# Kernel tuning notes

Hardware: AMD Instinct MI355X
Metric: run time of the kernel (lower is better)

The kernel has to match this reference:

```python
import jax, jax.numpy as jnp
import numpy as np

EPS = 1e-8
N_ITER = 3
S = 8      # n_slots
D = 64     # slot_size
HID = 128  # mlp hidden


def _ln(x, w, b):
    m = jnp.mean(x, axis=-1, keepdims=True)
    v = jnp.var(x, axis=-1, keepdims=True)
    return (x - m) * jax.lax.rsqrt(v + 1e-5) * w + b


def setup_inputs() -> dict:
    key = jax.random.key(0)
    ks = jax.random.split(key, 20)
    B, N, Din = 128, 4096, 64
    g = lambda k, sh, s: (jax.random.normal(k, sh, jnp.float32) * s)
    return {
        "inputs": jax.random.normal(ks[0], (B, N, Din), jnp.float32),
        "eps_noise": jax.random.normal(ks[1], (B, S, D), jnp.float32),
        "slot_mu": g(ks[2], (1, 1, D), 0.1),
        "slot_logvar": g(ks[3], (1, 1, D), 0.1),
        "k_w": g(ks[4], (D, Din), 1.0 / np.sqrt(Din)),
        "v_w": g(ks[5], (D, Din), 1.0 / np.sqrt(Din)),
        "q_w": g(ks[6], (D, D), 1.0 / np.sqrt(D)),
        "ni_w": jnp.ones((Din,), jnp.float32), "ni_b": jnp.zeros((Din,), jnp.float32),
        "ns_w": jnp.ones((D,), jnp.float32),  "ns_b": jnp.zeros((D,), jnp.float32),
        "nr_w": jnp.ones((D,), jnp.float32),  "nr_b": jnp.zeros((D,), jnp.float32),
        "gru_wih": g(ks[7], (3 * D, D), 1.0 / np.sqrt(D)),
        "gru_whh": g(ks[8], (3 * D, D), 1.0 / np.sqrt(D)),
        "gru_bih": jnp.zeros((3 * D,), jnp.float32),
        "gru_bhh": jnp.zeros((3 * D,), jnp.float32),
        "mlp_w1": g(ks[9], (HID, D), 1.0 / np.sqrt(D)),
        "mlp_w2": g(ks[10], (D, HID), 1.0 / np.sqrt(HID)),
        "mlp_b2": jnp.zeros((D,), jnp.float32),
    }


def _gru(x, h, wih, whh, bih, bhh):
    gi = x @ wih.T + bih  # [BS, 3D]
    gh = h @ whh.T + bhh
    i_r, i_z, i_n = jnp.split(gi, 3, axis=-1)
    h_r, h_z, h_n = jnp.split(gh, 3, axis=-1)
    r = jax.nn.sigmoid(i_r + h_r)
    z = jax.nn.sigmoid(i_z + h_z)
    n = jnp.tanh(i_n + r * h_n)
    return (1.0 - z) * n + z * h


def _step(slots, k, v, q_w, ns_w, ns_b, nr_w, nr_b,
          gru_wih, gru_whh, gru_bih, gru_bhh, mlp_w1, mlp_w2, mlp_b2):
    B = slots.shape[0]
    q = _ln(slots, ns_w, ns_b) @ q_w.T                     # [B,S,D]
    logits = jnp.einsum('bnd,bsd->bns', k, q)              # [B,N,S]
    w = jax.nn.softmax(logits, axis=-1) + EPS              # softmax over slots
    w = w / jnp.sum(w, axis=-2, keepdims=True)             # renorm over tokens
    atten_maps = jnp.einsum('bns,bnd->bsd', w, v)          # [B,S,D]
    h = _gru(atten_maps.reshape(B * S, D), slots.reshape(B * S, D),
             gru_wih, gru_whh, gru_bih, gru_bhh)
    h = h + (jax.nn.relu(_ln(h, nr_w, nr_b) @ mlp_w1.T) @ mlp_w2.T + mlp_b2)
    return h.reshape(B, S, D), w


def reference(inputs, eps_noise, slot_mu, slot_logvar, k_w, v_w, q_w,
              ni_w, ni_b, ns_w, ns_b, nr_w, nr_b,
              gru_wih, gru_whh, gru_bih, gru_bhh, mlp_w1, mlp_w2, mlp_b2):
    std = jnp.exp(0.5 * slot_logvar)
    slots = slot_mu + std * eps_noise                      # [B,S,D]
    x = _ln(inputs, ni_w, ni_b)
    k = (x @ k_w.T) / np.sqrt(D).astype(np.float32)        # [B,N,D]
    v = x @ v_w.T
    args = (q_w, ns_w, ns_b, nr_w, nr_b, gru_wih, gru_whh,
            gru_bih, gru_bhh, mlp_w1, mlp_w2, mlp_b2)
    for _ in range(N_ITER):
        slots, w = _step(slots, k, v, *args)
    slots, w = _step(jax.lax.stop_gradient(slots), k, v, *args)
    return slots, w
```

## Files before the change

kernel.cpp:

```cpp
#include <hip/hip_runtime.h>
#include <hip/hip_bf16.h>

#define BB 128
#define NN 4096
#define DD 64
#define SS 8
#define HH 128

typedef __attribute__((ext_vector_type(8))) short short8;
typedef __attribute__((ext_vector_type(4))) short short4v;
typedef __attribute__((ext_vector_type(4))) float f32x4;

__device__ __forceinline__ float warp_red_sum(float v) {
    #pragma unroll
    for (int off = 32; off; off >>= 1) v += __shfl_xor(v, off);
    return v;
}

__device__ __forceinline__ float bcastlane(float v, int l) {
    return __int_as_float(__builtin_amdgcn_readlane(__float_as_int(v), l));
}

__device__ __forceinline__ unsigned short bfu(float f) {
    __hip_bfloat16 h = __float2bfloat16(f);
    return *(unsigned short*)&h;
}

__device__ __forceinline__ unsigned pk2(float a, float b) {
    return (unsigned)bfu(a) | ((unsigned)bfu(b) << 16);
}

__device__ __forceinline__ short4v ds_tr16(unsigned off) {
    short4v r;
    asm volatile("ds_read_b64_tr_b16 %0, %1" : "=v"(r) : "v"(off));
    return r;
}

__device__ __forceinline__ void ln_block(
    const float* __restrict__ inp, const float* __restrict__ niw,
    const float* __restrict__ nib, unsigned short* __restrict__ xb,
    int tok0, int tid)
{
    const int lane = tid & 63, widx = tid >> 6;
    const int t8 = lane >> 3, d8 = lane & 7;
    const float4 wn0 = *(const float4*)&niw[d8 * 8];
    const float4 wn1 = *(const float4*)&niw[d8 * 8 + 4];
    const float4 bn0 = *(const float4*)&nib[d8 * 8];
    const float4 bn1 = *(const float4*)&nib[d8 * 8 + 4];
    #pragma unroll
    for (int it = 0; it < 4; ++it) {
        const int m = widx * 32 + it * 8 + t8;
        const float* rowp = inp + (size_t)(tok0 + m) * 64 + d8 * 8;
        float4 a = *(const float4*)rowp;
        float4 c = *(const float4*)(rowp + 4);
        float s1 = (a.x + a.y + a.z + a.w) + (c.x + c.y + c.z + c.w);
        float s2 = fmaf(a.x, a.x, fmaf(a.y, a.y, fmaf(a.z, a.z, a.w * a.w)));
        s2 = fmaf(c.x, c.x, fmaf(c.y, c.y, fmaf(c.z, c.z, fmaf(c.w, c.w, s2))));
        #pragma unroll
        for (int o = 1; o < 8; o <<= 1) { s1 += __shfl_xor(s1, o); s2 += __shfl_xor(s2, o); }
        float mean = s1 * (1.0f / 64.0f);
        float var = s2 * (1.0f / 64.0f) - mean * mean;
        float rstd = rsqrtf(var + 1e-5f);
        float y[8];
        y[0] = (a.x - mean) * rstd * wn0.x + bn0.x;
        y[1] = (a.y - mean) * rstd * wn0.y + bn0.y;
        y[2] = (a.z - mean) * rstd * wn0.z + bn0.z;
        y[3] = (a.w - mean) * rstd * wn0.w + bn0.w;
        y[4] = (c.x - mean) * rstd * wn1.x + bn1.x;
        y[5] = (c.y - mean) * rstd * wn1.y + bn1.y;
        y[6] = (c.z - mean) * rstd * wn1.z + bn1.z;
        y[7] = (c.w - mean) * rstd * wn1.w + bn1.w;
        uint4 o4;
        o4.x = pk2(y[0], y[1]); o4.y = pk2(y[2], y[3]);
        o4.z = pk2(y[4], y[5]); o4.w = pk2(y[6], y[7]);
        *(uint4*)&xb[(size_t)(tok0 + m) * 64 + d8 * 8] = o4;
    }
}

__device__ __forceinline__ void gru_core(
    float nx, float dt, int row, int lane,
    const float* __restrict__ vwT, const float* __restrict__ wihT,
    const float* __restrict__ whhT, const float* __restrict__ w1T,
    const float* __restrict__ w2T, const float* __restrict__ bih,
    const float* __restrict__ bhh, const float* __restrict__ nrw,
    const float* __restrict__ nrb, const float* __restrict__ b2,
    const float* __restrict__ qwT, const float* __restrict__ k_w,
    const float* __restrict__ nsw, const float* __restrict__ nsb,
    const float* __restrict__ slotsIn, float* __restrict__ slotsOut,
    unsigned short* __restrict__ qb)
{
    float xp = 0.f;
    #pragma unroll 8
    for (int i = 0; i < 64; ++i) xp = fmaf(bcastlane(nx, i), vwT[i * 64 + lane], xp);
    float x = xp / dt;
    float h = slotsIn[row * 64 + lane];
    float air = 0, aiz = 0, ain = 0, ahr = 0, ahz = 0, ahn = 0;
    #pragma unroll 8
    for (int i = 0; i < 64; ++i) {
        float xi = bcastlane(x, i), hi = bcastlane(h, i);
        const float* wi = wihT + i * 192;
        const float* wh = whhT + i * 192;
        air = fmaf(xi, wi[lane], air);
        aiz = fmaf(xi, wi[64 + lane], aiz);
        ain = fmaf(xi, wi[128 + lane], ain);
        ahr = fmaf(hi, wh[lane], ahr);
        ahz = fmaf(hi, wh[64 + lane], ahz);
        ahn = fmaf(hi, wh[128 + lane], ahn);
    }
    air += bih[lane]; aiz += bih[64 + lane]; ain += bih[128 + lane];
    ahr += bhh[lane]; ahz += bhh[64 + lane]; ahn += bhh[128 + lane];
    float r = 1.f / (1.f + __expf(-(air + ahr)));
    float z = 1.f / (1.f + __expf(-(aiz + ahz)));
    float n = tanhf(ain + r * ahn);
    float hn = (1.f - z) * n + z * h;
    float m = warp_red_sum(hn) * (1.0f / 64.0f);
    float dx = hn - m;
    float var = warp_red_sum(dx * dx) * (1.0f / 64.0f);
    float u = dx * rsqrtf(var + 1e-5f) * nrw[lane] + nrb[lane];
    float o0 = 0.f, o1 = 0.f;
    #pragma unroll 8
    for (int i = 0; i < 64; ++i) {
        float ui = bcastlane(u, i);
        const float* w1r = w1T + i * 128;
        o0 = fmaf(ui, w1r[lane], o0);
        o1 = fmaf(ui, w1r[64 + lane], o1);
    }
    o0 = fmaxf(o0, 0.f); o1 = fmaxf(o1, 0.f);
    float y = 0.f;
    #pragma unroll 8
    for (int j = 0; j < 64; ++j) y = fmaf(bcastlane(o0, j), w2T[j * 64 + lane], y);
    #pragma unroll 8
    for (int j = 0; j < 64; ++j) y = fmaf(bcastlane(o1, j), w2T[(64 + j) * 64 + lane], y);
    y += b2[lane];
    float out = hn + y;
    slotsOut[row * 64 + lane] = out;
    float m2 = warp_red_sum(out) * (1.0f / 64.0f);
    float dx2 = out - m2;
    float var2 = warp_red_sum(dx2 * dx2) * (1.0f / 64.0f);
    float u2 = dx2 * rsqrtf(var2 + 1e-5f) * nsw[lane] + nsb[lane];
    float q = 0.f;
    #pragma unroll 8
    for (int i = 0; i < 64; ++i) q = fmaf(bcastlane(u2, i), qwT[i * 64 + lane], q);
    float qp = 0.f;
    #pragma unroll 8
    for (int o = 0; o < 64; ++o) qp = fmaf(bcastlane(q, o), k_w[o * 64 + lane], qp);
    qb[row * 64 + lane] = bfu(qp * 0.125f);
}

__global__ __launch_bounds__(256) void fused_pre(
    const float* __restrict__ inp, const float* __restrict__ niw, const float* __restrict__ nib,
    const float* __restrict__ eps, const float* __restrict__ mu, const float* __restrict__ lv,
    const float* __restrict__ q_w, const float* __restrict__ k_w,
    const float* __restrict__ nsw, const float* __restrict__ nsb,
    const float* __restrict__ v_w, const float* __restrict__ wih, const float* __restrict__ whh,
    const float* __restrict__ w1, const float* __restrict__ w2,
    unsigned short* __restrict__ xb, unsigned short* __restrict__ qb,
    float* __restrict__ slots,
    float* __restrict__ vwT, float* __restrict__ qwT,
    float* __restrict__ wihT, float* __restrict__ whhT,
    float* __restrict__ w1T, float* __restrict__ w2T)
{
    const int bid = blockIdx.x, tid = threadIdx.x;
    const int lane = tid & 63, widx = tid >> 6;
    if (bid < 64) {
        int i0 = bid * 256 + tid, nthr = 16384;
        for (int t = i0; t < 4096; t += nthr) {
            int i = t >> 6, o = t & 63;
            vwT[t] = v_w[o * 64 + i];
            qwT[t] = q_w[o * 64 + i];
        }
        for (int t = i0; t < 12288; t += nthr) {
            int r = t / 192, c = t % 192;
            wihT[t] = wih[c * 64 + r];
            whhT[t] = whh[c * 64 + r];
        }
        for (int t = i0; t < 8192; t += nthr) {
            int r = t >> 7, c = t & 127;
            w1T[t] = w1[c * 64 + r];
        }
        for (int t = i0; t < 8192; t += nthr) {
            int r = t >> 6, c = t & 63;
            w2T[t] = w2[c * 128 + r];
        }
    }
    ln_block(inp, niw, nib, xb, bid * 128, tid);
    if (bid >= 64 && bid < 320) {
        const int row = (bid - 64) * 4 + widx;
        const int idx = row * 64 + lane;
        float s0 = mu[lane] + __expf(0.5f * lv[lane]) * eps[idx];
        slots[idx] = s0;
        float m = warp_red_sum(s0) * (1.0f / 64.0f);
        float dx = s0 - m;
        float var = warp_red_sum(dx * dx) * (1.0f / 64.0f);
        float xln = dx * rsqrtf(var + 1e-5f) * nsw[lane] + nsb[lane];
        float q = 0.f;
        #pragma unroll 8
        for (int i = 0; i < 64; ++i) q = fmaf(bcastlane(xln, i), q_w[lane * 64 + i], q);
        float qp = 0.f;
        #pragma unroll 8
        for (int o = 0; o < 64; ++o) qp = fmaf(bcastlane(q, o), k_w[o * 64 + lane], qp);
        qb[idx] = bfu(qp * 0.125f);
    }
}

__global__ __launch_bounds__(256) void attn_mfma(
    const __hip_bfloat16* __restrict__ xb,
    const unsigned short* __restrict__ qb,
    float* __restrict__ numerP, float* __restrict__ denomP, float* __restrict__ wout)
{
    __shared__ unsigned short smem[11904];
    unsigned short* Qs = smem;
    const int tid = threadIdx.x, lane = tid & 63, widx = tid >> 6;
    unsigned short* wls = smem + 1152 + widx * 640;
    unsigned short* Xw  = smem + 3712 + widx * 2048;
    const int b = blockIdx.y;
    const int quad = lane >> 4, l16 = lane & 15;
    const int twave0 = blockIdx.x * 512 + widx * 128;

    short8 bkA[2][2], bkB[2][2];
    #pragma unroll
    for (int t4h = 0; t4h < 2; ++t4h) {
        const size_t xrow = ((size_t)b * NN + twave0 + t4h * 16 + l16) * 64;
        bkA[t4h][0] = *(const short8*)&xb[xrow + quad * 8];
        bkA[t4h][1] = *(const short8*)&xb[xrow + 32 + quad * 8];
    }

    for (int t = tid; t < 1024; t += 256) {
        int s = t >> 6, dd = t & 63;
        Qs[s * 72 + dd] = (s < 8) ? qb[b * 512 + t] : (unsigned short)0;
    }
    for (int t = lane; t < 320; t += 64) wls[320 + t] = 0;
    __syncthreads();

    short8 aq0 = *(const short8*)&Qs[l16 * 72 + quad * 8];
    short8 aq1 = *(const short8*)&Qs[l16 * 72 + 32 + quad * 8];

    f32x4 accv[4];
    #pragma unroll
    for (int nt = 0; nt < 4; ++nt) accv[nt] = (f32x4){0.f, 0.f, 0.f, 0.f};
    float dacc[4] = {0.f, 0.f, 0.f, 0.f};

    unsigned short* xw0 = Xw + (quad >> 1) * 512 + l16 * 16 + (quad & 1) * 8;
    const unsigned xtr = (unsigned)(size_t)Xw
                       + (unsigned)((quad * 8 + (l16 >> 2)) * 32 + (l16 & 3) * 8);

    auto PROC = [&](short8 (&cur)[2][2], short8 (&nxt)[2][2], int hg, bool pf) {
        const int t0g = twave0 + hg * 32;
        if (pf) {
            #pragma unroll
            for (int t4h = 0; t4h < 2; ++t4h) {
                const size_t xrow = ((size_t)b * NN + t0g + 32 + t4h * 16 + l16) * 64;
                nxt[t4h][0] = *(const short8*)&xb[xrow + quad * 8];
                nxt[t4h][1] = *(const short8*)&xb[xrow + 32 + quad * 8];
            }
        }
        #pragma unroll
        for (int t4h = 0; t4h < 2; ++t4h) {
            const int tok = t0g + t4h * 16 + l16;
            short8 bk0 = cur[t4h][0];
            short8 bk1 = cur[t4h][1];
            *(short8*)(xw0 + t4h * 256) = bk0;
            *(short8*)(xw0 + t4h * 256 + 1024) = bk1;
            f32x4 lg = (f32x4){0.f, 0.f, 0.f, 0.f};
            lg = __builtin_amdgcn_mfma_f32_16x16x32_bf16(aq0, bk0, lg, 0, 0, 0);
            lg = __builtin_amdgcn_mfma_f32_16x16x32_bf16(aq1, bk1, lg, 0, 0, 0);
            float e[4];
            #pragma unroll
            for (int r = 0; r < 4; ++r) e[r] = __expf(lg[r]);
            float s4 = (e[0] + e[1]) + (e[2] + e[3]);
            float stot = s4 + __shfl_xor(s4, 16);
            float rs = __builtin_amdgcn_rcpf(stot);
            float wv[4];
            #pragma unroll
            for (int r = 0; r < 4; ++r) { wv[r] = fmaf(e[r], rs, 1e-8f); dacc[r] += wv[r]; }
            if (quad < 2) {
                #pragma unroll
                for (int r = 0; r < 4; ++r)
                    wls[(quad * 4 + r) * 40 + t4h * 16 + l16] = bfu(wv[r]);
                if (wout)
                    *(float4*)&wout[((size_t)b * NN + tok) * 8 + quad * 4] =
                        make_float4(wv[0], wv[1], wv[2], wv[3]);
            }
        }
        asm volatile("" ::: "memory");
        short8 aw = *(const short8*)&wls[l16 * 40 + quad * 8];
        short4v rlo[4], rhi[4];
        #pragma unroll
        for (int nt = 0; nt < 4; ++nt) {
            rlo[nt] = ds_tr16(xtr + nt * 1024);
            rhi[nt] = ds_tr16(xtr + nt * 1024 + 128);
        }
        asm volatile("s_waitcnt lgkmcnt(0)");
        __builtin_amdgcn_sched_barrier(0);
        #pragma unroll
        for (int nt = 0; nt < 4; ++nt) {
            short8 bv = __builtin_shufflevector(rlo[nt], rhi[nt], 0, 1, 2, 3, 4, 5, 6, 7);
            accv[nt] = __builtin_amdgcn_mfma_f32_16x16x32_bf16(aw, bv, accv[nt], 0, 0, 0);
        }
    };

    PROC(bkA, bkB, 0, true);
    PROC(bkB, bkA, 1, true);
    PROC(bkA, bkB, 2, true);
    PROC(bkB, bkA, 3, false);

    #pragma unroll
    for (int r = 0; r < 4; ++r) {
        dacc[r] += __shfl_xor(dacc[r], 1);
        dacc[r] += __shfl_xor(dacc[r], 2);
        dacc[r] += __shfl_xor(dacc[r], 4);
        dacc[r] += __shfl_xor(dacc[r], 8);
    }
    __syncthreads();
    float* red = (float*)smem;
    float* dred = red + 2048;
    if (quad < 2) {
        #pragma unroll
        for (int nt = 0; nt < 4; ++nt)
            #pragma unroll
            for (int r = 0; r < 4; ++r)
                red[widx * 512 + (quad * 4 + r) * 64 + nt * 16 + l16] = accv[nt][r];
        if (l16 == 0) {
            #pragma unroll
            for (int r = 0; r < 4; ++r) dred[widx * 8 + quad * 4 + r] = dacc[r];
        }
    }
    __syncthreads();
    float* np = numerP + ((size_t)b * 8 + blockIdx.x) * 512;
    for (int e = tid; e < 512; e += 256)
        np[e] = red[e] + red[512 + e] + red[1024 + e] + red[1536 + e];
    if (tid < 8)
        denomP[((size_t)b * 8 + blockIdx.x) * 8 + tid] =
            dred[tid] + dred[8 + tid] + dred[16 + tid] + dred[24 + tid];
}

__global__ __launch_bounds__(256) void gru_q_kernel(
    const float* __restrict__ numerP, const float* __restrict__ denomP,
    const float* __restrict__ slotsIn,
    const float* __restrict__ vwT, const float* __restrict__ wihT, const float* __restrict__ whhT,
    const float* __restrict__ w1T, const float* __restrict__ w2T,
    const float* __restrict__ bih, const float* __restrict__ bhh,
    const float* __restrict__ nrw, const float* __restrict__ nrb,
    const float* __restrict__ b2,
    const float* __restrict__ qwT, const float* __restrict__ k_w,
    const float* __restrict__ nsw, const float* __restrict__ nsb,
    float* __restrict__ slotsOut, unsigned short* __restrict__ qb,
    float* __restrict__ denomF)
{
    const int tid = threadIdx.x, lane = tid & 63;
    const int row = blockIdx.x * 4 + (tid >> 6);
    const int bb = row >> 3, ss = row & 7;
    float nx = 0.f, dt = 0.f;
    #pragma unroll
    for (int xx = 0; xx < 8; ++xx) {
        nx += numerP[((size_t)bb * 8 + xx) * 512 + ss * 64 + lane];
        dt += denomP[((size_t)bb * 8 + xx) * 8 + ss];
    }
    if (lane == 0) denomF[row] = dt;
    gru_core(nx, dt, row, lane, vwT, wihT, whhT, w1T, w2T, bih, bhh, nrw, nrb, b2,
             qwT, k_w, nsw, nsb, slotsIn, slotsOut, qb);
}

__global__ __launch_bounds__(256) void renorm_kernel(float* __restrict__ wout,
                                                     const float* __restrict__ denom)
{
    const size_t i4 = (size_t)blockIdx.x * blockDim.x + threadIdx.x;
    const size_t b = i4 >> 13;
    const int half = (int)(i4 & 1);
    float4 v = reinterpret_cast<float4*>(wout)[i4];
    const float4 dv = reinterpret_cast<const float4*>(denom)[b * 2 + half];
    v.x /= dv.x; v.y /= dv.y; v.z /= dv.z; v.w /= dv.w;
    reinterpret_cast<float4*>(wout)[i4] = v;
}

extern "C" void kernel_launch(void* const* d_in, const int* in_sizes, int n_in,
                              void* d_out, int out_size, void* d_ws, size_t ws_size,
                              hipStream_t stream)
{
    const float* inputs  = (const float*)d_in[0];
    const float* eps_n   = (const float*)d_in[1];
    const float* mu      = (const float*)d_in[2];
    const float* lv      = (const float*)d_in[3];
    const float* k_w     = (const float*)d_in[4];
    const float* v_w     = (const float*)d_in[5];
    const float* q_w     = (const float*)d_in[6];
    const float* ni_w    = (const float*)d_in[7];
    const float* ni_b    = (const float*)d_in[8];
    const float* ns_w    = (const float*)d_in[9];
    const float* ns_b    = (const float*)d_in[10];
    const float* nr_w    = (const float*)d_in[11];
    const float* nr_b    = (const float*)d_in[12];
    const float* gru_wih = (const float*)d_in[13];
    const float* gru_whh = (const float*)d_in[14];
    const float* gru_bih = (const float*)d_in[15];
    const float* gru_bhh = (const float*)d_in[16];
    const float* mlp_w1  = (const float*)d_in[17];
    const float* mlp_w2  = (const float*)d_in[18];
    const float* mlp_b2  = (const float*)d_in[19];

    char* wsb = (char*)d_ws;
    unsigned short* xb  = (unsigned short*)wsb;
    float* P      = (float*)(wsb + 67108864);
    float* numerP = P;
    float* denomP = P + 524288;
    float* denomF = P + 532480;
    float* f      = (float*)(wsb + 134217728);
    float* slotsA = f;
    float* slotsB = f + 65536;
    unsigned short* qb = (unsigned short*)(f + 131072);
    float* vwT    = f + 296960;
    float* qwT    = f + 301056;
    float* wihT   = f + 305152;
    float* whhT   = f + 317440;
    float* w1T    = f + 329728;
    float* w2T    = f + 337920;

    float* out_slots = (float*)d_out;
    float* out_w     = out_slots + 65536;

    fused_pre<<<4096, 256, 0, stream>>>(inputs, ni_w, ni_b, eps_n, mu, lv,
                                        q_w, k_w, ns_w, ns_b,
                                        v_w, gru_wih, gru_whh, mlp_w1, mlp_w2,
                                        xb, qb, slotsA,
                                        vwT, qwT, wihT, whhT, w1T, w2T);

    float* cur = slotsA;
    for (int step = 0; step < 4; ++step) {
        attn_mfma<<<dim3(8, 128), 256, 0, stream>>>((const __hip_bfloat16*)xb, qb,
                                                    numerP, denomP,
                                                    step == 3 ? out_w : nullptr);
        float* nxt = (step == 3) ? out_slots : ((step & 1) ? slotsA : slotsB);
        gru_q_kernel<<<256, 256, 0, stream>>>(numerP, denomP, cur,
                                              vwT, wihT, whhT, w1T, w2T,
                                              gru_bih, gru_bhh, nr_w, nr_b, mlp_b2,
                                              qwT, k_w, ns_w, ns_b,
                                              nxt, qb, denomF);
        cur = nxt;
    }
    renorm_kernel<<<4096, 256, 0, stream>>>(out_w, denomF);
}
```

Before: 378.8 us.

## Fuse GRU update into attention kernel via last-block-per-batch atomic counter

Merges the per-step attention and GRU/query kernels into one templated kernel. Each block publishes its partial numerator and denominator with agent-scope stores, then bumps a per-batch, per-step counter. The last of the 8 blocks for a batch reduces the partials and runs the GRU, MLP and next-query update. This removes four kernel launches and their inter-kernel gaps, and also drops the shared-memory Q staging and its barrier by loading Q straight from global memory. In exchange it adds serial tail work on one block per batch and relies on fences and atomics for correctness.

```diff
diff --git a/kernel.cpp b/kernel.cpp
--- a/kernel.cpp
+++ b/kernel.cpp
@@ -28,6 +28,13 @@
 
 __device__ __forceinline__ unsigned pk2(float a, float b) {
     return (unsigned)bfu(a) | ((unsigned)bfu(b) << 16);
+}
+
+__device__ __forceinline__ void store_agent(float* p, float v) {
+    __hip_atomic_store(p, v, __ATOMIC_RELAXED, __HIP_MEMORY_SCOPE_AGENT);
+}
+__device__ __forceinline__ float load_agent(const float* p) {
+    return __hip_atomic_load(p, __ATOMIC_RELAXED, __HIP_MEMORY_SCOPE_AGENT);
 }
 
 __device__ __forceinline__ short4v ds_tr16(unsigned off) {
@@ -158,7 +165,8 @@
     float* __restrict__ slots,
     float* __restrict__ vwT, float* __restrict__ qwT,
     float* __restrict__ wihT, float* __restrict__ whhT,
-    float* __restrict__ w1T, float* __restrict__ w2T)
+    float* __restrict__ w1T, float* __restrict__ w2T,
+    int* __restrict__ counters)
 {
     const int bid = blockIdx.x, tid = threadIdx.x;
     const int lane = tid & 63, widx = tid >> 6;
@@ -182,6 +190,9 @@
             int r = t >> 6, c = t & 63;
             w2T[t] = w2[c * 128 + r];
         }
+    }
+    if (bid == 320) {
+        for (int t = tid; t < 512; t += 256) counters[t] = 0;
     }
     ln_block(inp, niw, nib, xb, bid * 128, tid);
     if (bid >= 64 && bid < 320) {
@@ -203,16 +214,28 @@
     }
 }
 
-__global__ __launch_bounds__(256) void attn_mfma(
+template<int STEP>
+__global__ __launch_bounds__(256) void fused_step(
     const __hip_bfloat16* __restrict__ xb,
-    const unsigned short* __restrict__ qb,
-    float* __restrict__ numerP, float* __restrict__ denomP, float* __restrict__ wout)
-{
-    __shared__ unsigned short smem[11904];
-    unsigned short* Qs = smem;
+    unsigned short* __restrict__ qb,
+    float* __restrict__ numerP, float* __restrict__ denomP,
+    float* __restrict__ wout, int* __restrict__ counters,
+    const float* __restrict__ slotsIn, float* __restrict__ slotsOut,
+    const float* __restrict__ vwT, const float* __restrict__ wihT,
+    const float* __restrict__ whhT, const float* __restrict__ w1T,
+    const float* __restrict__ w2T,
+    const float* __restrict__ bih, const float* __restrict__ bhh,
+    const float* __restrict__ nrw, const float* __restrict__ nrb,
+    const float* __restrict__ b2,
+    const float* __restrict__ qwT, const float* __restrict__ k_w,
+    const float* __restrict__ nsw, const float* __restrict__ nsb,
+    float* __restrict__ denomF)
+{
+    __shared__ unsigned short smem[10752];
+    __shared__ int sflag;
     const int tid = threadIdx.x, lane = tid & 63, widx = tid >> 6;
-    unsigned short* wls = smem + 1152 + widx * 640;
-    unsigned short* Xw  = smem + 3712 + widx * 2048;
+    unsigned short* wls = smem + widx * 640;
+    unsigned short* Xw  = smem + 2560 + widx * 2048;
     const int b = blockIdx.y;
     const int quad = lane >> 4, l16 = lane & 15;
     const int twave0 = blockIdx.x * 512 + widx * 128;
@@ -225,15 +248,13 @@
         bkA[t4h][1] = *(const short8*)&xb[xrow + 32 + quad * 8];
     }
 
-    for (int t = tid; t < 1024; t += 256) {
-        int s = t >> 6, dd = t & 63;
-        Qs[s * 72 + dd] = (s < 8) ? qb[b * 512 + t] : (unsigned short)0;
+    short8 aq0 = (short8){0, 0, 0, 0, 0, 0, 0, 0};
+    short8 aq1 = (short8){0, 0, 0, 0, 0, 0, 0, 0};
+    if (l16 < 8) {
+        aq0 = *(const short8*)&qb[b * 512 + l16 * 64 + quad * 8];
+        aq1 = *(const short8*)&qb[b * 512 + l16 * 64 + 32 + quad * 8];
     }
     for (int t = lane; t < 320; t += 64) wls[320 + t] = 0;
-    __syncthreads();
-
-    short8 aq0 = *(const short8*)&Qs[l16 * 72 + quad * 8];
-    short8 aq1 = *(const short8*)&Qs[l16 * 72 + 32 + quad * 8];
 
     f32x4 accv[4];
     #pragma unroll
@@ -277,7 +298,7 @@
                 #pragma unroll
                 for (int r = 0; r < 4; ++r)
                     wls[(quad * 4 + r) * 40 + t4h * 16 + l16] = bfu(wv[r]);
-                if (wout)
+                if (STEP == 3)
                     *(float4*)&wout[((size_t)b * NN + tok) * 8 + quad * 4] =
                         make_float4(wv[0], wv[1], wv[2], wv[3]);
             }
@@ -328,37 +349,36 @@
     __syncthreads();
     float* np = numerP + ((size_t)b * 8 + blockIdx.x) * 512;
     for (int e = tid; e < 512; e += 256)
-        np[e] = red[e] + red[512 + e] + red[1024 + e] + red[1536 + e];
+        store_agent(&np[e], red[e] + red[512 + e] + red[1024 + e] + red[1536 + e]);
     if (tid < 8)
-        denomP[((size_t)b * 8 + blockIdx.x) * 8 + tid] =
-            dred[tid] + dred[8 + tid] + dred[16 + tid] + dred[24 + tid];
-}
-
-__global__ __launch_bounds__(256) void gru_q_kernel(
-    const float* __restrict__ numerP, const float* __restrict__ denomP,
-    const float* __restrict__ slotsIn,
-    const float* __restrict__ vwT, const float* __restrict__ wihT, const float* __restrict__ whhT,
-    const float* __restrict__ w1T, const float* __restrict__ w2T,
-    const float* __restrict__ bih, const float* __restrict__ bhh,
-    const float* __restrict__ nrw, const float* __restrict__ nrb,
-    const float* __restrict__ b2,
-    const float* __restrict__ qwT, const float* __restrict__ k_w,
-    const float* __restrict__ nsw, const float* __restrict__ nsb,
-    float* __restrict__ slotsOut, unsigned short* __restrict__ qb,
-    float* __restrict__ denomF)
-{
-    const int tid = threadIdx.x, lane = tid & 63;
-    const int row = blockIdx.x * 4 + (tid >> 6);
-    const int bb = row >> 3, ss = row & 7;
-    float nx = 0.f, dt = 0.f;
-    #pragma unroll
-    for (int xx = 0; xx < 8; ++xx) {
-        nx += numerP[((size_t)bb * 8 + xx) * 512 + ss * 64 + lane];
-        dt += denomP[((size_t)bb * 8 + xx) * 8 + ss];
-    }
-    if (lane == 0) denomF[row] = dt;
-    gru_core(nx, dt, row, lane, vwT, wihT, whhT, w1T, w2T, bih, bhh, nrw, nrb, b2,
-             qwT, k_w, nsw, nsb, slotsIn, slotsOut, qb);
+        store_agent(&denomP[((size_t)b * 8 + blockIdx.x) * 8 + tid],
+                    dred[tid] + dred[8 + tid] + dred[16 + tid] + dred[24 + tid]);
+
+    __threadfence();
+    __syncthreads();
+    if (tid == 0) {
+        int old = atomicAdd(&counters[STEP * 128 + b], 1);
+        sflag = (old == 7) ? 1 : 0;
+    }
+    __syncthreads();
+    if (sflag) {
+        __threadfence();
+        #pragma unroll
+        for (int rr = 0; rr < 2; ++rr) {
+            const int row = b * 8 + widx * 2 + rr;
+            const int ss = row & 7;
+            float nx = 0.f, dt = 0.f;
+            #pragma unroll
+            for (int xx = 0; xx < 8; ++xx) {
+                nx += load_agent(&numerP[((size_t)b * 8 + xx) * 512 + ss * 64 + lane]);
+                dt += load_agent(&denomP[((size_t)b * 8 + xx) * 8 + ss]);
+            }
+            if (lane == 0) denomF[row] = dt;
+            gru_core(nx, dt, row, lane, vwT, wihT, whhT, w1T, w2T,
+                     bih, bhh, nrw, nrb, b2, qwT, k_w, nsw, nsb,
+                     slotsIn, slotsOut, qb);
+        }
+    }
 }
 
 __global__ __launch_bounds__(256) void renorm_kernel(float* __restrict__ wout,
@@ -368,7 +388,7 @@
     const size_t b = i4 >> 13;
     const int half = (int)(i4 & 1);
     float4 v = reinterpret_cast<float4*>(wout)[i4];
-    const float4 dv = reinterpret_cast<const float4*>(denom)[b * 2 + half];
+    const float4 dv = *(const float4*)&denom[b * 8 + half * 4];
     v.x /= dv.x; v.y /= dv.y; v.z /= dv.z; v.w /= dv.w;
     reinterpret_cast<float4*>(wout)[i4] = v;
 }
@@ -404,6 +424,7 @@
     float* numerP = P;
     float* denomP = P + 524288;
     float* denomF = P + 532480;
+    int*   counters = (int*)(P + 533504);
     float* f      = (float*)(wsb + 134217728);
     float* slotsA = f;
     float* slotsB = f + 65536;
@@ -422,20 +443,20 @@
                                         q_w, k_w, ns_w, ns_b,
                                         v_w, gru_wih, gru_whh, mlp_w1, mlp_w2,
                                         xb, qb, slotsA,
-                                        vwT, qwT, wihT, whhT, w1T, w2T);
-
-    float* cur = slotsA;
-    for (int step = 0; step < 4; ++step) {
-        attn_mfma<<<dim3(8, 128), 256, 0, stream>>>((const __hip_bfloat16*)xb, qb,
-                                                    numerP, denomP,
-                                                    step == 3 ? out_w : nullptr);
-        float* nxt = (step == 3) ? out_slots : ((step & 1) ? slotsA : slotsB);
-        gru_q_kernel<<<256, 256, 0, stream>>>(numerP, denomP, cur,
-                                              vwT, wihT, whhT, w1T, w2T,
-                                              gru_bih, gru_bhh, nr_w, nr_b, mlp_b2,
-                                              qwT, k_w, ns_w, ns_b,
-                                              nxt, qb, denomF);
-        cur = nxt;
-    }
+                                        vwT, qwT, wihT, whhT, w1T, w2T, counters);
+
+    #define LAUNCH_STEP(S, SIN, SOUT)                                              \
+        fused_step<S><<<dim3(8, 128), 256, 0, stream>>>(                           \
+            (const __hip_bfloat16*)xb, qb, numerP, denomP, out_w, counters,        \
+            SIN, SOUT, vwT, wihT, whhT, w1T, w2T,                                  \
+            gru_bih, gru_bhh, nr_w, nr_b, mlp_b2,                                  \
+            qwT, k_w, ns_w, ns_b, denomF)
+
+    LAUNCH_STEP(0, slotsA, slotsB);
+    LAUNCH_STEP(1, slotsB, slotsA);
+    LAUNCH_STEP(2, slotsA, slotsB);
+    LAUNCH_STEP(3, slotsB, out_slots);
+    #undef LAUNCH_STEP
+
     renorm_kernel<<<4096, 256, 0, stream>>>(out_w, denomF);
 }
```

After: 961.3 us. 2.54x slower.
